# Kernel tuning notes

Measured on AMD Instinct MI355X. Metric: run time of the kernel, lower is better.

The kernel has to match this reference:

```python
import jax, jax.numpy as jnp
import numpy as np
from jax import lax

PRE_NMS_TOP_N = 2000
POST_NMS_TOP_N = 1000
NMS_THRESH = 0.7
MIN_SIZE = 0.0
BBOX_XFORM_CLIP = float(np.log(1000.0 / 16.0))
NEG = jnp.float32(-1e30)


def setup_inputs() -> dict:
    key = jax.random.key(0)
    k1, k2, k3, k4, k5 = jax.random.split(key, 5)
    N, A, H, W = 16, 3, 256, 336
    img_h, img_w = 1024, 1344
    num = A * H * W  # 258048 anchors per image
    objectness = jax.random.normal(k1, (N, A, H, W), jnp.float32)
    box_regression = jax.random.normal(k2, (N, A * 4, H, W), jnp.float32) * 0.5
    # synthetic but valid xyxy anchors (x2 > x1, y2 > y1)
    cx = jax.random.uniform(k3, (N, num)) * img_w
    cy = jax.random.uniform(k4, (N, num)) * img_h
    wh = 16.0 + jax.random.uniform(k5, (N, num, 2)) * 256.0
    anchors = jnp.stack([cx - 0.5 * wh[..., 0], cy - 0.5 * wh[..., 1],
                         cx + 0.5 * wh[..., 0], cy + 0.5 * wh[..., 1]], axis=-1)
    return {"anchors": anchors.astype(jnp.float32), "objectness": objectness,
            "box_regression": box_regression, "img_h": img_h, "img_w": img_w}


def box_decode(codes, anchors):
    # BoxCoder(weights=(1,1,1,1)).decode, TO_REMOVE=1 convention
    w = anchors[..., 2] - anchors[..., 0] + 1.0
    h = anchors[..., 3] - anchors[..., 1] + 1.0
    ctr_x = anchors[..., 0] + 0.5 * w
    ctr_y = anchors[..., 1] + 0.5 * h
    dx, dy, dw, dh = codes[..., 0], codes[..., 1], codes[..., 2], codes[..., 3]
    dw = jnp.minimum(dw, BBOX_XFORM_CLIP)
    dh = jnp.minimum(dh, BBOX_XFORM_CLIP)
    pcx = dx * w + ctr_x
    pcy = dy * h + ctr_y
    pw = jnp.exp(dw) * w
    ph = jnp.exp(dh) * h
    return jnp.stack([pcx - 0.5 * pw, pcy - 0.5 * ph,
                      pcx + 0.5 * pw - 1.0, pcy + 0.5 * ph - 1.0], axis=-1)


def pairwise_iou(boxes):
    area = (boxes[:, 2] - boxes[:, 0] + 1.0) * (boxes[:, 3] - boxes[:, 1] + 1.0)
    lt = jnp.maximum(boxes[:, None, :2], boxes[None, :, :2])  # [K,K,2]
    rb = jnp.minimum(boxes[:, None, 2:], boxes[None, :, 2:])
    wh = jnp.maximum(rb - lt + 1.0, 0.0)
    inter = wh[..., 0] * wh[..., 1]
    return inter / (area[:, None] + area[None, :] - inter)


def nms_keep(boxes, valid):
    # boxes already sorted by score desc; greedy suppression scan over rows
    K = boxes.shape[0]
    iou = pairwise_iou(boxes)  # [K,K]
    idx = jnp.arange(K)

    def body(keep, xs):
        row, i = xs
        sup = keep[i] & (idx > i) & (row > NMS_THRESH)
        return keep & ~sup, None

    keep, _ = lax.scan(body, valid, (iou, idx))
    return keep


def reference(anchors, objectness, box_regression, img_h, img_w):
    N, A, H, W = objectness.shape
    # permute_and_flatten: (N,A,H,W) -> (N, H*W*A)
    obj = jax.nn.sigmoid(jnp.transpose(objectness, (0, 2, 3, 1)).reshape(N, -1))
    breg = jnp.transpose(box_regression.reshape(N, A, 4, H, W), (0, 3, 4, 1, 2)).reshape(N, -1, 4)
    k = min(PRE_NMS_TOP_N, obj.shape[1])
    scores, topk_idx = lax.top_k(obj, k)  # sorted desc
    batch = jnp.arange(N)[:, None]
    breg = breg[batch, topk_idx]        # [N,k,4]
    anc = anchors[batch, topk_idx]      # [N,k,4]
    boxes = box_decode(breg, anc)       # [N,k,4]
    # clip_to_image (TO_REMOVE=1)
    x1 = jnp.clip(boxes[..., 0], 0.0, img_w - 1)
    y1 = jnp.clip(boxes[..., 1], 0.0, img_h - 1)
    x2 = jnp.clip(boxes[..., 2], 0.0, img_w - 1)
    y2 = jnp.clip(boxes[..., 3], 0.0, img_h - 1)
    boxes = jnp.stack([x1, y1, x2, y2], axis=-1)
    # remove_small_boxes as a validity mask (fixed shape)
    ws = x2 - x1 + 1.0
    hs = y2 - y1 + 1.0
    valid = (ws >= MIN_SIZE) & (hs >= MIN_SIZE)
    keep = jax.vmap(nms_keep)(boxes, valid)  # [N,k]
    masked = jnp.where(keep, scores, NEG)
    final_scores, sel = lax.top_k(masked, POST_NMS_TOP_N)  # preserves score order
    final_boxes = boxes[batch, sel]
    # [N, post_nms_top_n, 5]: xyxy + objectness (padded slots have score ~ -1e30)
    return jnp.concatenate([final_boxes, final_scores[..., None]], axis=-1)
```

## Files before the change

### kernel.cpp

```cpp
#include <hip/hip_runtime.h>
#include <stdint.h>

#define NIMG 16
#define AANCH 3
#define HH 256
#define WW 336
#define HWP (HH*WW)
#define NUM (AANCH*HWP)
#define TOTAL (NIMG*NUM)
#define PRE_K 2000
#define POST_K 1000
#define NMS_TH 0.7f
#define NEGV -1e30f
#define CAND_CAP 4096
#define ROWS 2048
#define RWORDS 64
#define CHUNK 4096
#define CBLOCKS (NUM / CHUNK)
#define HPARTS 16
#define HBINS 4096
#define HCHUNK (NUM / HPARTS)

#define WS_HIST 0u
#define WS_COLT 0u
#define WS_CBOX 262144u
#define WS_CSCO 1310720u
#define WS_CUT  4194304u
#define WS_CNT  4194560u
#define WS_CAND 4194816u
#define WS_BOX  4719104u
#define WS_SCO  5243392u
#define WS_RMI  5374464u
#define WS_SEL  5378560u
#define WS_MASK 5444096u

__device__ __forceinline__ uint32_t fkey(float f){
    uint32_t b = __float_as_uint(f);
    return (b & 0x80000000u) ? ~b : (b | 0x80000000u);
}
__device__ __forceinline__ float keyf(uint32_t k){
    uint32_t b = (k & 0x80000000u) ? (k & 0x7FFFFFFFu) : ~k;
    return __uint_as_float(b);
}

__global__ __launch_bounds__(1024) void k_hist(const float* __restrict__ obj,
                                               uint32_t* __restrict__ part,
                                               uint32_t* __restrict__ cnt,
                                               uint32_t* __restrict__ rminit){
    int img = blockIdx.x >> 4;
    int blk = blockIdx.x & 15;
    int tid = threadIdx.x;
    if (blockIdx.x == 0){
        for (int i = tid; i < 32 + NIMG * RWORDS; i += 1024){
            if (i < 32) cnt[i] = 0u;
            else        rminit[i - 32] = 0u;
        }
    }
    __shared__ uint32_t h[HBINS];
    #pragma unroll
    for (int i = 0; i < HBINS / 1024; ++i) h[tid + i * 1024] = 0u;
    __syncthreads();
    const float* base = obj + (size_t)img * NUM + (size_t)blk * HCHUNK;
    for (int e = tid * 4; e < HCHUNK; e += 4096){
        float4 v = *(const float4*)(base + e);
        atomicAdd(&h[fkey(v.x) >> 20], 1u);
        atomicAdd(&h[fkey(v.y) >> 20], 1u);
        atomicAdd(&h[fkey(v.z) >> 20], 1u);
        atomicAdd(&h[fkey(v.w) >> 20], 1u);
    }
    __syncthreads();
    uint32_t* p = part + ((size_t)blockIdx.x) * HBINS;
    #pragma unroll
    for (int i = 0; i < HBINS / 1024; ++i) p[tid + i * 1024] = h[tid + i * 1024];
}

__global__ __launch_bounds__(1024) void k_binsel(const uint32_t* __restrict__ part,
                                                 uint32_t* __restrict__ cut,
                                                 uint32_t* __restrict__ nAout){
    int img = blockIdx.x, tid = threadIdx.x;
    const uint32_t* pb = part + (size_t)img * HPARTS * HBINS;
    int bin0 = HBINS - 4 * (tid + 1);
    uint32_t c0 = 0, c1 = 0, c2 = 0, c3 = 0;
    for (int k = 0; k < HPARTS; ++k){
        const uint4 v = *(const uint4*)(pb + (size_t)k * HBINS + bin0);
        c0 += v.x; c1 += v.y; c2 += v.z; c3 += v.w;
    }
    uint32_t s = c0 + c1 + c2 + c3;
    __shared__ uint32_t ss[1024];
    uint32_t x = s;
    ss[tid] = x; __syncthreads();
    for (int d = 1; d < 1024; d <<= 1){
        uint32_t y = (tid >= d) ? ss[tid - d] : 0u;
        __syncthreads();
        x += y; ss[tid] = x;
        __syncthreads();
    }
    uint32_t incl = x, excl = x - s;
    if (excl < PRE_K && incl >= PRE_K){
        uint32_t c = excl;
        uint32_t cc[4] = {c0, c1, c2, c3};
        for (int j = 3; j >= 0; --j){
            uint32_t cb = c;
            c += cc[j];
            if (c >= PRE_K){
                cut[img] = ((uint32_t)(bin0 + j)) << 20;
                nAout[img] = cb;
                break;
            }
        }
    }
}

__device__ __forceinline__ void emit_candidate(
        uint32_t key, uint32_t f, uint32_t pos, int img,
        const float* __restrict__ anchors, const float* __restrict__ breg,
        float imw, float imh,
        unsigned long long* __restrict__ cand,
        float4* __restrict__ cboxes, float* __restrict__ cscores){
    const float CLIPV = 4.135166556742356f;
    cand[img * CAND_CAP + pos] = ((unsigned long long)key << 32)
        | ((unsigned long long)((~f) & 0x3FFFFu) << 14) | (unsigned long long)pos;
    float logit = keyf(key);
    float sc = 1.0f / (1.0f + expf(-logit));
    const float* an = anchors + ((size_t)img * NUM + f) * 4;
    float ax1 = an[0], ay1 = an[1], ax2 = an[2], ay2 = an[3];
    int a = (int)(f % AANCH); int hw = (int)(f / AANCH);
    size_t bbase = ((size_t)img * 12 + a * 4) * HWP + (size_t)hw;
    float dx = breg[bbase], dy = breg[bbase + HWP];
    float dw = breg[bbase + 2 * (size_t)HWP], dh = breg[bbase + 3 * (size_t)HWP];
    float aw = ax2 - ax1 + 1.0f, ah = ay2 - ay1 + 1.0f;
    float cx = ax1 + 0.5f * aw, cy = ay1 + 0.5f * ah;
    dw = fminf(dw, CLIPV); dh = fminf(dh, CLIPV);
    float pcx = dx * aw + cx, pcy = dy * ah + cy;
    float pw = expf(dw) * aw, ph = expf(dh) * ah;
    float x1 = pcx - 0.5f * pw, y1 = pcy - 0.5f * ph;
    float x2 = pcx + 0.5f * pw - 1.0f, y2 = pcy + 0.5f * ph - 1.0f;
    x1 = fminf(fmaxf(x1, 0.0f), imw - 1.0f);
    y1 = fminf(fmaxf(y1, 0.0f), imh - 1.0f);
    x2 = fminf(fmaxf(x2, 0.0f), imw - 1.0f);
    y2 = fminf(fmaxf(y2, 0.0f), imh - 1.0f);
    bool valid = ((x2 - x1 + 1.0f) >= 0.0f) && ((y2 - y1 + 1.0f) >= 0.0f);
    cboxes[img * CAND_CAP + pos] = make_float4(x1, y1, x2, y2);
    cscores[img * CAND_CAP + pos] = valid ? sc : -sc;
}

__global__ __launch_bounds__(256) void k_compact(const float* __restrict__ obj,
                                                 const uint32_t* __restrict__ cut,
                                                 const uint32_t* __restrict__ nAarr,
                                                 uint32_t* __restrict__ cnt,
                                                 unsigned long long* __restrict__ cand,
                                                 const float* __restrict__ anchors,
                                                 const float* __restrict__ breg,
                                                 const int* __restrict__ pimh,
                                                 const int* __restrict__ pimw,
                                                 float4* __restrict__ cboxes,
                                                 float* __restrict__ cscores){
    int img   = blockIdx.x / CBLOCKS;
    int chunk = blockIdx.x - img * CBLOCKS;
    int base  = img * NUM + chunk * CHUNK;
    __shared__ uint32_t lcA, lcB, gbA, gbB;
    __shared__ uint2 lbuf[CHUNK];
    if (threadIdx.x == 0){ lcA = 0u; lcB = 0u; }
    __syncthreads();
    uint32_t cutv = cut[img];
    uint32_t cutbin = cutv >> 20;
    float4 v[4];
    #pragma unroll
    for (int it = 0; it < 4; ++it)
        v[it] = *(const float4*)(obj + base + it * 1024 + (int)threadIdx.x * 4);
    #pragma unroll
    for (int it = 0; it < 4; ++it){
        int e = it * 1024 + (int)threadIdx.x * 4;
        float vv[4] = {v[it].x, v[it].y, v[it].z, v[it].w};
        #pragma unroll
        for (int q = 0; q < 4; ++q){
            uint32_t k = fkey(vv[q]);
            if (k >= cutv){
                int r = chunk * CHUNK + e + q;
                int a = r / HWP, hw = r - a * HWP;
                uint32_t f = (uint32_t)(hw * AANCH + a);
                if ((k >> 20) > cutbin){
                    uint32_t p = atomicAdd(&lcA, 1u);
                    lbuf[p] = make_uint2(k, f);
                } else {
                    uint32_t p = atomicAdd(&lcB, 1u);
                    lbuf[CHUNK - 1 - p] = make_uint2(k, f);
                }
            }
        }
    }
    __syncthreads();
    if (threadIdx.x == 0){
        gbA = (lcA > 0u) ? atomicAdd(&cnt[img], lcA) : 0u;
        gbB = (lcB > 0u) ? atomicAdd(&cnt[16 + img], lcB) : 0u;
    }
    __syncthreads();
    uint32_t nA  = nAarr[img];
    uint32_t nAp = (nA + 1u) & ~1u;
    float imw = (float)(*pimw), imh = (float)(*pimh);
    uint32_t na = lcA, ga = gbA, nb = lcB, gb = gbB;
    for (uint32_t t = threadIdx.x; t < na; t += 256u){
        uint32_t pos = ga + t;
        uint2 kf = lbuf[t];
        emit_candidate(kf.x, kf.y, pos, img, anchors, breg, imw, imh,
                       cand, cboxes, cscores);
    }
    for (uint32_t t = threadIdx.x; t < nb; t += 256u){
        uint32_t pos = nAp + gb + t;
        if (pos < CAND_CAP){
            uint2 kf = lbuf[CHUNK - 1 - t];
            emit_candidate(kf.x, kf.y, pos, img, anchors, breg, imw, imh,
                           cand, cboxes, cscores);
        }
    }
}

__global__ __launch_bounds__(256) void k_rank(
        const unsigned long long* __restrict__ cand, const uint32_t* __restrict__ cnt,
        const uint32_t* __restrict__ nAarr,
        const float4* __restrict__ cboxes, const float* __restrict__ cscores,
        float4* __restrict__ boxes_s, float* __restrict__ scores_s,
        uint32_t* __restrict__ rminit){
    int img = blockIdx.x >> 4;
    int b   = blockIdx.x & 15;
    int tid = threadIdx.x;
    int e   = b * 256 + tid;
    uint32_t nA   = nAarr[img];
    uint32_t nAp  = (nA + 1u) & ~1u;
    uint32_t nB   = min(cnt[16 + img], (uint32_t)CAND_CAP - nAp);
    uint32_t end  = nAp + nB;
    uint32_t endp = (end + 1u) & ~1u;
    const unsigned long long* cp = cand + img * CAND_CAP;
    __shared__ alignas(16) unsigned long long tile[CAND_CAP];
    for (int i = tid; i < (int)endp; i += 256){
        bool v = (i < (int)nA) || (i >= (int)nAp && i < (int)end);
        tile[i] = v ? cp[i] : 0ull;
    }
    __syncthreads();
    bool inA = e < (int)nA;
    bool inB = (e >= (int)nAp) && (e < (int)end);
    bool validE = inA || inB;
    unsigned long long mine = validE ? tile[e] : ~0ull;
    int s0 = inA ? 0 : (inB ? (int)(nAp >> 1) : 0);
    int s1 = inA ? (int)(nAp >> 1) : (inB ? (int)(endp >> 1) : 0);
    int rank = inB ? (int)nA : 0;
    const ulonglong2* tile2 = (const ulonglong2*)tile;
    #pragma unroll 8
    for (int i = s0; i < s1; ++i){
        ulonglong2 p = tile2[i];
        rank += (p.x > mine) ? 1 : 0;
        rank += (p.y > mine) ? 1 : 0;
    }
    if (validE && rank < PRE_K){
        float4 bx = cboxes[img * CAND_CAP + e];
        float s   = cscores[img * CAND_CAP + e];
        boxes_s[img * ROWS + rank] = bx;
        scores_s[img * ROWS + rank] = fabsf(s);
        if (s < 0.0f) atomicOr(&rminit[img * RWORDS + (rank >> 5)], 1u << (rank & 31));
    }
}

__global__ __launch_bounds__(64) void k_diag(const float4* __restrict__ boxes_s,
                                             unsigned long long* __restrict__ colT){
    int img = blockIdx.x >> 5;
    int b   = blockIdx.x & 31;
    int j   = threadIdx.x;
    __shared__ float4 B[64];
    __shared__ float  AR[64];
    float4 bj = boxes_s[img * ROWS + b * 64 + j];
    float aj = (bj.z - bj.x + 1.0f) * (bj.w - bj.y + 1.0f);
    B[j] = bj; AR[j] = aj;
    __syncthreads();
    unsigned long long col = 0ull;
    #pragma unroll 8
    for (int i = 0; i < 64; ++i){
        float4 bi = B[i]; float ai = AR[i];
        float xx1 = fmaxf(bi.x, bj.x), yy1 = fmaxf(bi.y, bj.y);
        float xx2 = fminf(bi.z, bj.z), yy2 = fminf(bi.w, bj.w);
        float iw = fmaxf(xx2 - xx1 + 1.0f, 0.0f);
        float ih = fmaxf(yy2 - yy1 + 1.0f, 0.0f);
        float inter = iw * ih;
        bool pred = (i < j) && (inter > NMS_TH * (ai + aj - inter));
        col |= pred ? (1ull << i) : 0ull;
    }
    colT[(size_t)(img * 32 + b) * 64 + j] = col;
}

__global__ __launch_bounds__(1024) void k_mask(const float4* __restrict__ boxes_s,
                                               uint32_t* __restrict__ mask){
    int img = blockIdx.x >> 4;
    int rc  = blockIdx.x & 15;
    int tid = threadIdx.x;
    int lane = tid & 63;
    int wv = tid >> 6;
    int gw = rc * 16 + wv;
    __shared__ float4 B[PRE_K];
    __shared__ float  AR[PRE_K];
    const float4* bp = boxes_s + img * ROWS;
    for (int t = tid; t < PRE_K; t += 1024){
        float4 b = bp[t]; B[t] = b;
        AR[t] = (b.z - b.x + 1.0f) * (b.w - b.y + 1.0f);
    }
    __syncthreads();
    uint32_t* M = mask + (size_t)img * ROWS * RWORDS;
    for (int i = gw; i < PRE_K; i += 256){
        float4 bi = B[i];
        float ai = AR[i];
        unsigned long long* Mrow = (unsigned long long*)(M + (size_t)i * RWORDS);
        for (int jb = (i >> 6); jb < 32; ++jb){
            int j = (jb << 6) + lane;
            bool pred = false;
            if (j > i && j < PRE_K){
                float4 bj = B[j];
                float xx1 = fmaxf(bi.x, bj.x), yy1 = fmaxf(bi.y, bj.y);
                float xx2 = fminf(bi.z, bj.z), yy2 = fminf(bi.w, bj.w);
                float iw = fmaxf(xx2 - xx1 + 1.0f, 0.0f);
                float ih = fmaxf(yy2 - yy1 + 1.0f, 0.0f);
                float inter = iw * ih;
                pred = inter > NMS_TH * (ai + AR[j] - inter);
            }
            unsigned long long bm = __ballot(pred);
            if (lane == 0) Mrow[jb] = bm;
        }
    }
}

__global__ __launch_bounds__(64, 1) void k_scan(const uint32_t* __restrict__ mask,
                                                const unsigned long long* __restrict__ colT,
                                                const uint32_t* __restrict__ rminit,
                                                const float4* __restrict__ boxes_s,
                                                const float* __restrict__ scores_s,
                                                float* __restrict__ out){
    int img = blockIdx.x; int lane = threadIdx.x;
    const uint32_t* M = mask + (size_t)img * ROWS * RWORDS;
    const unsigned long long* CT = colT + (size_t)img * 32 * 64;
    __shared__ uint32_t S[POST_K];
    uint32_t rm = rminit[img * RWORDS + lane];
    if (lane == 62) rm |= 0xFFFF0000u;
    if (lane == 63) rm  = 0xFFFFFFFFu;

    uint32_t rowsA[64], rowsB[64];
    unsigned long long colA, colB;
    {
        const uint32_t* Mb = M + lane;
        colA = CT[lane];
        #pragma unroll
        for (int i = 0; i < 64; ++i) rowsA[i] = Mb[(size_t)i * RWORDS];
    }

#define PHASE(B, ROWSX, COLX)                                                   \
    {                                                                           \
        uint32_t lo = __shfl(rm, 2 * (B)), hi = __shfl(rm, 2 * (B) + 1);        \
        unsigned long long inc = ((unsigned long long)hi << 32)                 \
                               | (unsigned long long)lo;                        \
        bool alivej = ((inc >> lane) & 1ull) == 0ull;                           \
        unsigned long long keep = ~inc;                                         \
        for (int it = 0; it < 66; ++it){                                        \
            bool ok = alivej && ((COLX & keep) == 0ull);                        \
            unsigned long long nk = __ballot(ok);                               \
            if (nk == keep) break;                                              \
            keep = nk;                                                          \
        }                                                                       \
        uint32_t acc = 0u;                                                      \
        _Pragma("unroll")                                                       \
        for (int i = 0; i < 64; ++i)                                            \
            acc |= (keep & (1ull << i)) ? ROWSX[i] : 0u;                        \
        rm |= (lane >= 2 * (B)) ? acc : 0u;                                     \
        unsigned long long rmb = ~keep;                                         \
        if (lane == 2 * (B))     rm = (uint32_t)rmb;                            \
        if (lane == 2 * (B) + 1) rm = (uint32_t)(rmb >> 32);                    \
    }

    #pragma unroll 1
    for (int b = 0; b < 32; b += 2){
        {
            const uint32_t* Mb = M + (size_t)((b + 1) * 64) * RWORDS + lane;
            colB = CT[(size_t)(b + 1) * 64 + lane];
            #pragma unroll
            for (int i = 0; i < 64; ++i) rowsB[i] = Mb[(size_t)i * RWORDS];
        }
        PHASE(b, rowsA, colA);
        if (b + 2 < 32){
            const uint32_t* Mb = M + (size_t)((b + 2) * 64) * RWORDS + lane;
            colA = CT[(size_t)(b + 2) * 64 + lane];
            #pragma unroll
            for (int i = 0; i < 64; ++i) rowsA[i] = Mb[(size_t)i * RWORDS];
        }
        PHASE(b + 1, rowsB, colB);
    }
#undef PHASE

    uint32_t inr = (lane < 62) ? 0xFFFFFFFFu : (lane == 62 ? 0x0000FFFFu : 0u);
    uint32_t kw = (~rm) & inr;
    uint32_t sw = rm & inr;
    uint32_t kc = __popc(kw);
    uint32_t x = kc;
    for (int d = 1; d < 64; d <<= 1){ uint32_t y = __shfl_up(x, d); if (lane >= d) x += y; }
    uint32_t kexcl = x - kc;
    uint32_t ktot = __shfl(x, 63);
    uint32_t m = kw; uint32_t r = 0;
    while (m){
        int b = __ffs(m) - 1;
        uint32_t slot = kexcl + r;
        if (slot < POST_K) S[slot] = (uint32_t)(lane * 32 + b) | 0x80000000u;
        m &= m - 1; ++r;
    }
    if (ktot < POST_K){
        uint32_t sc2 = __popc(sw);
        uint32_t x2 = sc2;
        for (int d = 1; d < 64; d <<= 1){ uint32_t y = __shfl_up(x2, d); if (lane >= d) x2 += y; }
        uint32_t sexcl = x2 - sc2;
        uint32_t m2 = sw; uint32_t r2 = 0;
        while (m2){
            int b = __ffs(m2) - 1;
            uint32_t slot = ktot + sexcl + r2;
            if (slot >= ktot && slot < POST_K) S[slot] = (uint32_t)(lane * 32 + b);
            m2 &= m2 - 1; ++r2;
        }
    }
    __syncthreads();
    const float4* bp = boxes_s + img * ROWS;
    const float* sp = scores_s + img * ROWS;
    float* o = out + (size_t)img * POST_K * 5;
    for (int s = lane; s < POST_K; s += 64){
        uint32_t v = S[s];
        uint32_t pos = v & 0x7FFFFFFFu;
        bool kept = (v >> 31) != 0;
        float4 bx = bp[pos];
        float sc = kept ? sp[pos] : NEGV;
        float* oo = o + s * 5;
        oo[0] = bx.x; oo[1] = bx.y; oo[2] = bx.z; oo[3] = bx.w; oo[4] = sc;
    }
}

extern "C" void kernel_launch(void* const* d_in, const int* in_sizes, int n_in,
                              void* d_out, int out_size, void* d_ws, size_t ws_size,
                              hipStream_t stream) {
    const float* anchors = (const float*)d_in[0];
    const float* obj     = (const float*)d_in[1];
    const float* breg    = (const float*)d_in[2];
    const int*   pimh    = (const int*)d_in[3];
    const int*   pimw    = (const int*)d_in[4];
    float* out = (float*)d_out;
    uint8_t* ws = (uint8_t*)d_ws;

    uint32_t*           part     = (uint32_t*)(ws + WS_HIST);
    unsigned long long* colT     = (unsigned long long*)(ws + WS_COLT);
    float4*             cboxes   = (float4*)(ws + WS_CBOX);
    float*              cscores  = (float*)(ws + WS_CSCO);
    uint32_t*           cut      = (uint32_t*)(ws + WS_CUT);
    uint32_t*           nAarr    = (uint32_t*)(ws + WS_CUT + 64);
    uint32_t*           cnt      = (uint32_t*)(ws + WS_CNT);
    unsigned long long* cand     = (unsigned long long*)(ws + WS_CAND);
    float4*             boxes_s  = (float4*)(ws + WS_BOX);
    float*              scores_s = (float*)(ws + WS_SCO);
    uint32_t*           rminit   = (uint32_t*)(ws + WS_RMI);
    uint32_t*           mask     = (uint32_t*)(ws + WS_MASK);

    k_hist<<<NIMG * HPARTS, 1024, 0, stream>>>(obj, part, cnt, rminit);
    k_binsel<<<NIMG, 1024, 0, stream>>>(part, cut, nAarr);
    k_compact<<<NIMG * CBLOCKS, 256, 0, stream>>>(obj, cut, nAarr, cnt, cand,
                                                  anchors, breg, pimh, pimw,
                                                  cboxes, cscores);
    k_rank<<<NIMG * 16, 256, 0, stream>>>(cand, cnt, nAarr, cboxes, cscores,
                                          boxes_s, scores_s, rminit);
    k_diag<<<NIMG * 32, 64, 0, stream>>>(boxes_s, colT);
    k_mask<<<NIMG * 16, 1024, 0, stream>>>(boxes_s, mask);
    k_scan<<<NIMG, 64, 0, stream>>>(mask, colT, rminit, boxes_s, scores_s, out);
}
```

Baseline: 149.0 us.

## Split NMS scan row loading and mask OR across four wavefronts

```diff
diff --git a/kernel.cpp b/kernel.cpp
--- a/kernel.cpp
+++ b/kernel.cpp
@@ -325,30 +325,38 @@
     }
 }
 
-__global__ __launch_bounds__(64, 1) void k_scan(const uint32_t* __restrict__ mask,
-                                                const unsigned long long* __restrict__ colT,
-                                                const uint32_t* __restrict__ rminit,
-                                                const float4* __restrict__ boxes_s,
-                                                const float* __restrict__ scores_s,
-                                                float* __restrict__ out){
-    int img = blockIdx.x; int lane = threadIdx.x;
+__global__ __launch_bounds__(256) void k_scan(const uint32_t* __restrict__ mask,
+                                              const unsigned long long* __restrict__ colT,
+                                              const uint32_t* __restrict__ rminit,
+                                              const float4* __restrict__ boxes_s,
+                                              const float* __restrict__ scores_s,
+                                              float* __restrict__ out){
+    int img = blockIdx.x;
+    int tid = threadIdx.x;
+    int lane = tid & 63;
+    int wv = tid >> 6;
     const uint32_t* M = mask + (size_t)img * ROWS * RWORDS;
     const unsigned long long* CT = colT + (size_t)img * 32 * 64;
     __shared__ uint32_t S[POST_K];
-    uint32_t rm = rminit[img * RWORDS + lane];
-    if (lane == 62) rm |= 0xFFFF0000u;
-    if (lane == 63) rm  = 0xFFFFFFFFu;
-
-    uint32_t rowsA[64], rowsB[64];
-    unsigned long long colA, colB;
-    {
-        const uint32_t* Mb = M + lane;
-        colA = CT[lane];
-        #pragma unroll
-        for (int i = 0; i < 64; ++i) rowsA[i] = Mb[(size_t)i * RWORDS];
-    }
-
-#define PHASE(B, ROWSX, COLX)                                                   \
+    __shared__ uint32_t acc_lds[4][64];
+    __shared__ unsigned long long keep_lds;
+
+    uint32_t rm = 0u;
+    if (wv == 0){
+        rm = rminit[img * RWORDS + lane];
+        if (lane == 62) rm |= 0xFFFF0000u;
+        if (lane == 63) rm  = 0xFFFFFFFFu;
+    }
+    unsigned long long colA = 0ull, colB = 0ull, rmb_sav = 0ull;
+    uint32_t rowsA[16], rowsB[16];
+
+#define PRELOAD(B, ROWSX)                                                       \
+    {                                                                           \
+        const uint32_t* Mb = M + (size_t)((B) * 64 + wv * 16) * RWORDS + lane;  \
+        _Pragma("unroll")                                                       \
+        for (int r = 0; r < 16; ++r) ROWSX[r] = Mb[(size_t)r * RWORDS];         \
+    }
+#define FIXED_POINT(B, COLX)                                                    \
     {                                                                           \
         uint32_t lo = __shfl(rm, 2 * (B)), hi = __shfl(rm, 2 * (B) + 1);        \
         unsigned long long inc = ((unsigned long long)hi << 32)                 \
@@ -357,72 +365,95 @@
         unsigned long long keep = ~inc;                                         \
         for (int it = 0; it < 66; ++it){                                        \
             bool ok = alivej && ((COLX & keep) == 0ull);                        \
-            unsigned long long nk = __ballot(ok);                               \
+            unsigned long long nk = __ballot(ok);                              \
             if (nk == keep) break;                                              \
             keep = nk;                                                          \
         }                                                                       \
+        if (lane == 0) keep_lds = keep;                                         \
+        rmb_sav = ~keep;                                                        \
+    }
+#define APPLY(ROWSX)                                                            \
+    {                                                                           \
+        unsigned long long kp = keep_lds;                                       \
         uint32_t acc = 0u;                                                      \
         _Pragma("unroll")                                                       \
-        for (int i = 0; i < 64; ++i)                                            \
-            acc |= (keep & (1ull << i)) ? ROWSX[i] : 0u;                        \
+        for (int r = 0; r < 16; ++r)                                            \
+            acc |= ((kp >> (wv * 16 + r)) & 1ull) ? ROWSX[r] : 0u;              \
+        acc_lds[wv][lane] = acc;                                                \
+    }
+#define FINISH(B)                                                               \
+    {                                                                           \
+        uint32_t acc = acc_lds[0][lane] | acc_lds[1][lane]                      \
+                     | acc_lds[2][lane] | acc_lds[3][lane];                     \
         rm |= (lane >= 2 * (B)) ? acc : 0u;                                     \
-        unsigned long long rmb = ~keep;                                         \
-        if (lane == 2 * (B))     rm = (uint32_t)rmb;                            \
-        if (lane == 2 * (B) + 1) rm = (uint32_t)(rmb >> 32);                    \
-    }
+        if (lane == 2 * (B))     rm = (uint32_t)rmb_sav;                        \
+        if (lane == 2 * (B) + 1) rm = (uint32_t)(rmb_sav >> 32);                \
+    }
+
+    PRELOAD(0, rowsA);
+    if (wv == 0) colA = CT[lane];
 
     #pragma unroll 1
     for (int b = 0; b < 32; b += 2){
-        {
-            const uint32_t* Mb = M + (size_t)((b + 1) * 64) * RWORDS + lane;
+        PRELOAD(b + 1, rowsB);
+        if (wv == 0){
             colB = CT[(size_t)(b + 1) * 64 + lane];
-            #pragma unroll
-            for (int i = 0; i < 64; ++i) rowsB[i] = Mb[(size_t)i * RWORDS];
-        }
-        PHASE(b, rowsA, colA);
+            FIXED_POINT(b, colA);
+        }
+        __syncthreads();
+        APPLY(rowsA);
+        __syncthreads();
+        if (wv == 0) FINISH(b);
         if (b + 2 < 32){
-            const uint32_t* Mb = M + (size_t)((b + 2) * 64) * RWORDS + lane;
-            colA = CT[(size_t)(b + 2) * 64 + lane];
-            #pragma unroll
-            for (int i = 0; i < 64; ++i) rowsA[i] = Mb[(size_t)i * RWORDS];
-        }
-        PHASE(b + 1, rowsB, colB);
-    }
-#undef PHASE
-
-    uint32_t inr = (lane < 62) ? 0xFFFFFFFFu : (lane == 62 ? 0x0000FFFFu : 0u);
-    uint32_t kw = (~rm) & inr;
-    uint32_t sw = rm & inr;
-    uint32_t kc = __popc(kw);
-    uint32_t x = kc;
-    for (int d = 1; d < 64; d <<= 1){ uint32_t y = __shfl_up(x, d); if (lane >= d) x += y; }
-    uint32_t kexcl = x - kc;
-    uint32_t ktot = __shfl(x, 63);
-    uint32_t m = kw; uint32_t r = 0;
-    while (m){
-        int b = __ffs(m) - 1;
-        uint32_t slot = kexcl + r;
-        if (slot < POST_K) S[slot] = (uint32_t)(lane * 32 + b) | 0x80000000u;
-        m &= m - 1; ++r;
-    }
-    if (ktot < POST_K){
-        uint32_t sc2 = __popc(sw);
-        uint32_t x2 = sc2;
-        for (int d = 1; d < 64; d <<= 1){ uint32_t y = __shfl_up(x2, d); if (lane >= d) x2 += y; }
-        uint32_t sexcl = x2 - sc2;
-        uint32_t m2 = sw; uint32_t r2 = 0;
-        while (m2){
-            int b = __ffs(m2) - 1;
-            uint32_t slot = ktot + sexcl + r2;
-            if (slot >= ktot && slot < POST_K) S[slot] = (uint32_t)(lane * 32 + b);
-            m2 &= m2 - 1; ++r2;
+            PRELOAD(b + 2, rowsA);
+            if (wv == 0) colA = CT[(size_t)(b + 2) * 64 + lane];
+        }
+        if (wv == 0) FIXED_POINT(b + 1, colB);
+        __syncthreads();
+        APPLY(rowsB);
+        __syncthreads();
+        if (wv == 0) FINISH(b + 1);
+    }
+#undef PRELOAD
+#undef FIXED_POINT
+#undef APPLY
+#undef FINISH
+
+    if (wv == 0){
+        uint32_t inr = (lane < 62) ? 0xFFFFFFFFu : (lane == 62 ? 0x0000FFFFu : 0u);
+        uint32_t kw = (~rm) & inr;
+        uint32_t sw = rm & inr;
+        uint32_t kc = __popc(kw);
+        uint32_t x = kc;
+        for (int d = 1; d < 64; d <<= 1){ uint32_t y = __shfl_up(x, d); if (lane >= d) x += y; }
+        uint32_t kexcl = x - kc;
+        uint32_t ktot = __shfl(x, 63);
+        uint32_t m = kw; uint32_t r = 0;
+        while (m){
+            int bb = __ffs(m) - 1;
+            uint32_t slot = kexcl + r;
+            if (slot < POST_K) S[slot] = (uint32_t)(lane * 32 + bb) | 0x80000000u;
+            m &= m - 1; ++r;
+        }
+        if (ktot < POST_K){
+            uint32_t sc2 = __popc(sw);
+            uint32_t x2 = sc2;
+            for (int d = 1; d < 64; d <<= 1){ uint32_t y = __shfl_up(x2, d); if (lane >= d) x2 += y; }
+            uint32_t sexcl = x2 - sc2;
+            uint32_t m2 = sw; uint32_t r2 = 0;
+            while (m2){
+                int bb = __ffs(m2) - 1;
+                uint32_t slot = ktot + sexcl + r2;
+                if (slot >= ktot && slot < POST_K) S[slot] = (uint32_t)(lane * 32 + bb);
+                m2 &= m2 - 1; ++r2;
+            }
         }
     }
     __syncthreads();
     const float4* bp = boxes_s + img * ROWS;
     const float* sp = scores_s + img * ROWS;
     float* o = out + (size_t)img * POST_K * 5;
-    for (int s = lane; s < POST_K; s += 64){
+    for (int s = tid; s < POST_K; s += 256){
         uint32_t v = S[s];
         uint32_t pos = v & 0x7FFFFFFFu;
         bool kept = (v >> 31) != 0;
@@ -466,5 +497,5 @@
                                           boxes_s, scores_s, rminit);
     k_diag<<<NIMG * 32, 64, 0, stream>>>(boxes_s, colT);
     k_mask<<<NIMG * 16, 1024, 0, stream>>>(boxes_s, mask);
-    k_scan<<<NIMG, 64, 0, stream>>>(mask, colT, rminit, boxes_s, scores_s, out);
-}
+    k_scan<<<NIMG, 256, 0, stream>>>(mask, colT, rminit, boxes_s, scores_s, out);
+}
```

After: 133.4 us. 1.12x faster.
